# Optimization experiments

Hardware: AMD Instinct MI355X
Metric: run time of the kernel (lower is better)

Reference implementation:

```python
import jax, jax.numpy as jnp
import numpy as np

N_NODES = 50000
N_EDGES = 800000
N_GRAPHS = 64
F_IN = 128
HEADS = 4
CH = 32
HID = HEADS * CH  # 128
N_CLASSES = 10
N_LAYERS = 3
NEG_SLOPE = 0.2


def setup_inputs() -> dict:
    key = jax.random.key(0)
    ks = jax.random.split(key, 12)
    x = jax.random.normal(ks[0], (N_NODES, F_IN), dtype=jnp.float32)
    edge_index = jax.random.randint(ks[1], (2, N_EDGES), 0, N_NODES, dtype=jnp.int64)
    batch = jnp.sort(jax.random.randint(ks[2], (N_NODES,), 0, N_GRAPHS, dtype=jnp.int64))
    s = 0.1
    Wl = jax.random.normal(ks[3], (N_LAYERS, F_IN, HID), dtype=jnp.float32) * s
    Wr = jax.random.normal(ks[4], (N_LAYERS, F_IN, HID), dtype=jnp.float32) * s
    bl = jax.random.normal(ks[5], (N_LAYERS, HID), dtype=jnp.float32) * s
    br = jax.random.normal(ks[6], (N_LAYERS, HID), dtype=jnp.float32) * s
    att = jax.random.normal(ks[7], (N_LAYERS, HEADS, CH), dtype=jnp.float32) * s
    bias = jax.random.normal(ks[8], (N_LAYERS, HID), dtype=jnp.float32) * s
    lin_w = jax.random.normal(ks[9], (HID, N_CLASSES), dtype=jnp.float32) * s
    lin_b = jax.random.normal(ks[10], (N_CLASSES,), dtype=jnp.float32) * s
    return {"x": x, "edge_index": edge_index, "batch": batch, "Wl": Wl, "Wr": Wr,
            "bl": bl, "br": br, "att": att, "bias": bias, "lin_w": lin_w, "lin_b": lin_b}


def gatv2_layer(x, Wl, Wr, bl, br, att, bias, src, dst):
    # x: [N, D_in] -> out: [N, HEADS*CH]
    n = x.shape[0]
    xl = (x @ Wl + bl).reshape(n, HEADS, CH)  # source transform
    xr = (x @ Wr + br).reshape(n, HEADS, CH)  # target transform
    # GATv2 edge scores: a^T LeakyReLU(W_l x_j + W_r x_i), per head
    e = jnp.einsum('ehc,hc->eh', jax.nn.leaky_relu(xl[src] + xr[dst], NEG_SLOPE), att)  # [E, H]
    # softmax over edges sharing the same destination node
    m = jax.ops.segment_max(e, dst, num_segments=n)
    ee = jnp.exp(e - m[dst])
    denom = jax.ops.segment_sum(ee, dst, num_segments=n)
    alpha = ee / denom[dst]  # [E, H]
    out = jax.ops.segment_sum(xl[src] * alpha[:, :, None], dst, num_segments=n)  # [N, H, C]
    return out.reshape(n, HID) + bias


def reference(x, edge_index, batch, Wl, Wr, bl, br, att, bias, lin_w, lin_b):
    n = x.shape[0]
    loop = jnp.arange(n, dtype=edge_index.dtype)
    src = jnp.concatenate([edge_index[0], loop])  # self loops (PyG default)
    dst = jnp.concatenate([edge_index[1], loop])
    h = x
    for l in range(N_LAYERS):
        h = jax.nn.elu(gatv2_layer(h, Wl[l], Wr[l], bl[l], br[l], att[l], bias[l], src, dst))
    # global mean pool over graphs
    sums = jax.ops.segment_sum(h, batch, num_segments=N_GRAPHS)
    cnt = jax.ops.segment_sum(jnp.ones((n,), h.dtype), batch, num_segments=N_GRAPHS)
    pooled = sums / jnp.maximum(cnt, 1.0)[:, None]
    logits = jax.nn.elu(pooled @ lin_w + lin_b)
    return jax.nn.log_softmax(logits, axis=1)
```

## Files before the change

kernel.cpp:

```cpp
#include <hip/hip_runtime.h>
#include <hip/hip_bf16.h>
#include <math.h>

#define N_NODES 50000
#define N_EDGES 800000
#define N_GRAPHS 64
#define HID 128
#define N_CLASSES 10
#define N_LAYERS 3
#define NEG_SLOPE 0.2f

#define NB 196
#define BCAP 5120
#define ACHUNK 4096

typedef __attribute__((ext_vector_type(8))) short short8;
typedef __attribute__((ext_vector_type(4))) float f32x4;

__device__ inline ushort f2bf(float f) {
    uint u = __builtin_bit_cast(uint, f);
    u += 0x7fffu + ((u >> 16) & 1u);
    return (ushort)(u >> 16);
}
__device__ inline uint pk2bf(float a, float b) {
    return (uint)f2bf(a) | ((uint)f2bf(b) << 16);
}
__device__ inline float bflo(uint v) { return __builtin_bit_cast(float, v << 16); }
__device__ inline float bfhi(uint v) { return __builtin_bit_cast(float, v & 0xffff0000u); }


__global__ __launch_bounds__(256) void setup_kernel(
    const float* __restrict__ x, uint* __restrict__ xb, int n,
    const float* __restrict__ Wl, const float* __restrict__ Wr,
    uint* __restrict__ wt, int wtot,
    const int* __restrict__ ei, int E,
    int* __restrict__ bptr, uint* __restrict__ bbuf,
    int xqb, int wb) {
    __shared__ int hcnt[256];
    __shared__ int hexcl[256];
    __shared__ int lofs[256];
    __shared__ int delta[256];
    __shared__ uint stage[ACHUNK];
    int t = threadIdx.x;
    int blk = blockIdx.x;

    if (blk < xqb) {
        int j = blk * 256 + t;
        if (j < n * 16) {
            const float4* xp = (const float4*)x + (size_t)j * 2;
            float4 a = xp[0], b = xp[1];
            uint4 o;
            o.x = pk2bf(a.x, a.y); o.y = pk2bf(a.z, a.w);
            o.z = pk2bf(b.x, b.y); o.w = pk2bf(b.z, b.w);
            ((uint4*)xb)[j] = o;
        }
        return;
    }
    blk -= xqb;
    if (blk < wb) {
        int i = blk * 256 + t;
        if (i >= wtot) return;
        int kp = i & 63;
        int nn = (i >> 6) & 255;
        int l  = i >> 14;
        const float* W = (nn < 128) ? Wl : Wr;
        int c = nn & 127;
        wt[i] = pk2bf(W[l * 16384 + (2 * kp) * 128 + c],
                      W[l * 16384 + (2 * kp + 1) * 128 + c]);
        return;
    }
    blk -= wb;
    int total = E + n;
    int base = blk * ACHUNK;
    int cntblk = min(ACHUNK, total - base);
    hcnt[t] = 0; lofs[t] = 0;
    __syncthreads();

    uint v[16]; int bk[16];
#pragma unroll
    for (int j = 0; j < 16; ++j) {
        int e = base + j * 256 + t;
        bk[j] = -1;
        if (e < total) {
            int s, d;
            if (e < E) { s = ei[e]; d = ei[E + e]; }
            else       { s = e - E; d = e - E; }
            v[j] = ((uint)s << 16) | (uint)d;
            bk[j] = d >> 8;
            atomicAdd(&hcnt[bk[j]], 1);
        }
    }
    __syncthreads();
    int hv = hcnt[t];
    __shared__ int stmp[256];
    stmp[t] = hv;
    __syncthreads();
    for (int off = 1; off < 256; off <<= 1) {
        int u = (t >= off) ? stmp[t - off] : 0;
        __syncthreads();
        stmp[t] += u;
        __syncthreads();
    }
    hexcl[t] = stmp[t] - hv;
    __syncthreads();
#pragma unroll
    for (int j = 0; j < 16; ++j) {
        if (bk[j] >= 0) {
            int pos = hexcl[bk[j]] + atomicAdd(&lofs[bk[j]], 1);
            stage[pos] = v[j];
        }
    }
    __syncthreads();
    if (t < NB) {
        int c = hcnt[t];
        int gb = c ? atomicAdd(&bptr[t], c) : 0;
        delta[t] = t * BCAP + gb - hexcl[t];
    }
    __syncthreads();
    for (int idx = t; idx < cntblk; idx += 256) {
        uint val = stage[idx];
        int b = (val >> 8) & 0xff;
        int tgt = delta[b] + idx;
        if (tgt < (b + 1) * BCAP) bbuf[tgt] = val;
    }
}


__device__ __forceinline__ void gemm_body(
    const ushort* __restrict__ A, const ushort* __restrict__ Wt,
    const float* __restrict__ bl, const float* __restrict__ br,
    ushort* __restrict__ xlb, ushort* __restrict__ xrb, int n, int bid, int tid) {
    int wv = tid >> 6;
    int lane = tid & 63;
    int q = lane >> 4, m16 = lane & 15;
    int m0 = bid * 64;

    short8 bf[4][4];
#pragma unroll
    for (int nt = 0; nt < 4; ++nt) {
        const ushort* wp = Wt + (size_t)(wv * 64 + nt * 16 + m16) * 128 + q * 8;
#pragma unroll
        for (int ks = 0; ks < 4; ++ks) bf[nt][ks] = *(const short8*)(wp + ks * 32);
    }
    const ushort* ap[4];
#pragma unroll
    for (int mt = 0; mt < 4; ++mt) {
        int r = m0 + mt * 16 + m16;
        if (r > n - 1) r = n - 1;
        ap[mt] = A + (size_t)r * 128 + q * 8;
    }

    f32x4 z = {0.f, 0.f, 0.f, 0.f};
    f32x4 acc[4][4];
#pragma unroll
    for (int mt = 0; mt < 4; ++mt)
#pragma unroll
        for (int nt = 0; nt < 4; ++nt) acc[mt][nt] = z;

#pragma unroll
    for (int ks = 0; ks < 4; ++ks) {
        short8 af[4];
#pragma unroll
        for (int mt = 0; mt < 4; ++mt) af[mt] = *(const short8*)(ap[mt] + ks * 32);
#pragma unroll
        for (int mt = 0; mt < 4; ++mt)
#pragma unroll
            for (int nt = 0; nt < 4; ++nt)
                acc[mt][nt] = __builtin_amdgcn_mfma_f32_16x16x32_bf16(
                    bf[nt][ks], af[mt], acc[mt][nt], 0, 0, 0);
    }

    ushort* outp = (wv >= 2) ? xrb : xlb;
    const float* bx = (wv >= 2) ? br : bl;
    int fb = (wv & 1) * 64;
#pragma unroll
    for (int nt = 0; nt < 4; ++nt) {
        int fcol = fb + nt * 16 + q * 4;
        float4 b4 = *(const float4*)&bx[fcol];
#pragma unroll
        for (int mt = 0; mt < 4; ++mt) {
            int m = m0 + mt * 16 + m16;
            if (m < n) {
                ushort4 pk;
                pk.x = f2bf(acc[mt][nt][0] + b4.x);
                pk.y = f2bf(acc[mt][nt][1] + b4.y);
                pk.z = f2bf(acc[mt][nt][2] + b4.z);
                pk.w = f2bf(acc[mt][nt][3] + b4.w);
                *(ushort4*)&outp[(size_t)m * 128 + fcol] = pk;
            }
        }
    }
}

__global__ __launch_bounds__(256) void csr_gemm0_kernel(
    const int* __restrict__ bptr, const uint* __restrict__ bbuf, int n,
    int* __restrict__ row_start, int* __restrict__ ssrc,
    const ushort* __restrict__ A, const ushort* __restrict__ Wt,
    const float* __restrict__ bl, const float* __restrict__ br,
    ushort* __restrict__ xlb, ushort* __restrict__ xrb) {
    int t = threadIdx.x;
    if (blockIdx.x >= NB) {
        gemm_body(A, Wt, bl, br, xlb, xrb, n, blockIdx.x - NB, t);
        return;
    }
    int b = blockIdx.x;
    __shared__ int sb[256], h[256], hx[256], lofs[256];
    int bv = (t < NB) ? min(bptr[t], BCAP) : 0;
    sb[t] = bv;
    __syncthreads();
    for (int off = 1; off < 256; off <<= 1) {
        int u = (t >= off) ? sb[t - off] : 0;
        __syncthreads();
        sb[t] += u;
        __syncthreads();
    }
    int cnt = min(bptr[b], BCAP);
    int base = sb[b] - cnt;
    if (b == NB - 1 && t == 0) row_start[n] = sb[NB - 1];
    h[t] = 0; lofs[t] = 0;
    __syncthreads();
    const uint* bp = bbuf + (size_t)b * BCAP;
    for (int k = t; k < cnt; k += 256) atomicAdd(&h[bp[k] & 255u], 1);
    __syncthreads();
    int hv = h[t];
    hx[t] = hv;
    __syncthreads();
    for (int off = 1; off < 256; off <<= 1) {
        int u = (t >= off) ? hx[t - off] : 0;
        __syncthreads();
        hx[t] += u;
        __syncthreads();
    }
    int excl = hx[t] - hv;
    int node = (b << 8) + t;
    if (node < n) row_start[node] = base + excl;
    __syncthreads();
    h[t] = excl;
    __syncthreads();
    for (int k = t; k < cnt; k += 256) {
        uint val = bp[k];
        int dl = val & 255u;
        int pos = base + h[dl] + atomicAdd(&lofs[dl], 1);
        ssrc[pos] = (int)((val & 0xffff0000u) >> 8);
    }
}

__global__ __launch_bounds__(256) void gemm_mfma(
    const ushort* __restrict__ A, const ushort* __restrict__ Wt,
    const float* __restrict__ bl, const float* __restrict__ br,
    ushort* __restrict__ xlb, ushort* __restrict__ xrb, int n) {
    gemm_body(A, Wt, bl, br, xlb, xrb, n, blockIdx.x, threadIdx.x);
}


#define EDGE_MATH(u, c0, c1, c2, c3, e)                                  \
    {                                                                    \
        float t_;                                                        \
        c0 = bflo(u.x); c1 = bfhi(u.x); c2 = bflo(u.y); c3 = bfhi(u.y);  \
        t_ = c0 + xr0; t_ = fmaxf(t_, 0.2f * t_); e  = atx * t_;         \
        t_ = c1 + xr1; t_ = fmaxf(t_, 0.2f * t_); e += aty * t_;         \
        t_ = c2 + xr2; t_ = fmaxf(t_, 0.2f * t_); e += atz * t_;         \
        t_ = c3 + xr3; t_ = fmaxf(t_, 0.2f * t_); e += atw * t_;         \
    }

__global__ __launch_bounds__(256) void attn_kernel(
    const uint* __restrict__ xlb, const uint* __restrict__ xrb,
    const float* __restrict__ att, const float* __restrict__ bias,
    const int* __restrict__ row_start, const int* __restrict__ ssrc,
    uint* __restrict__ hout, int n) {
    int wave = threadIdx.x >> 6;
    int lane = threadIdx.x & 63;
    int half = lane >> 5;
    int l32  = lane & 31;
    int i = blockIdx.x * 4 + wave;
    if (i >= n) return;

    const char* xlB = (const char*)xlb;
    int lofs = l32 * 8;

    uint2 xru = *(const uint2*)((const char*)xrb + (size_t)i * 256 + lofs);
    float xr0 = bflo(xru.x), xr1 = bfhi(xru.x), xr2 = bflo(xru.y), xr3 = bfhi(xru.y);
    const float L2E = 1.4426950408889634f;
    float4 at = ((const float4*)att)[l32];
    float atx = at.x * L2E, aty = at.y * L2E, atz = at.z * L2E, atw = at.w * L2E;

    int p0 = row_start[i], p1 = row_start[i + 1];

    float den0 = 0.f, den1 = 0.f;
    float b00 = 0.f, b01 = 0.f, b02 = 0.f, b03 = 0.f;
    float b10 = 0.f, b11 = 0.f, b12 = 0.f, b13 = 0.f;

    int p = p0;
    for (; p + 8 <= p1; p += 8) {
        uint s0 = (uint)ssrc[p + half];
        uint s1 = (uint)ssrc[p + 2 + half];
        uint s2 = (uint)ssrc[p + 4 + half];
        uint s3 = (uint)ssrc[p + 6 + half];
        uint2 u0 = *(const uint2*)(xlB + (size_t)s0 + lofs);
        uint2 u1 = *(const uint2*)(xlB + (size_t)s1 + lofs);
        uint2 u2 = *(const uint2*)(xlB + (size_t)s2 + lofs);
        uint2 u3 = *(const uint2*)(xlB + (size_t)s3 + lofs);
        float c00, c01, c02, c03, c10, c11, c12, c13;
        float c20, c21, c22, c23, c30, c31, c32, c33;
        float e0, e1, e2, e3;
        EDGE_MATH(u0, c00, c01, c02, c03, e0);
        EDGE_MATH(u1, c10, c11, c12, c13, e1);
        EDGE_MATH(u2, c20, c21, c22, c23, e2);
        EDGE_MATH(u3, c30, c31, c32, c33, e3);
        e0 += __shfl_xor(e0, 1); e1 += __shfl_xor(e1, 1);
        e2 += __shfl_xor(e2, 1); e3 += __shfl_xor(e3, 1);
        e0 += __shfl_xor(e0, 2); e1 += __shfl_xor(e1, 2);
        e2 += __shfl_xor(e2, 2); e3 += __shfl_xor(e3, 2);
        e0 += __shfl_xor(e0, 4); e1 += __shfl_xor(e1, 4);
        e2 += __shfl_xor(e2, 4); e3 += __shfl_xor(e3, 4);
        float w0 = exp2f(e0), w1 = exp2f(e1), w2 = exp2f(e2), w3 = exp2f(e3);
        den0 += w0 + w2; den1 += w1 + w3;
        b00 += w0 * c00; b01 += w0 * c01; b02 += w0 * c02; b03 += w0 * c03;
        b10 += w1 * c10; b11 += w1 * c11; b12 += w1 * c12; b13 += w1 * c13;
        b00 += w2 * c20; b01 += w2 * c21; b02 += w2 * c22; b03 += w2 * c23;
        b10 += w3 * c30; b11 += w3 * c31; b12 += w3 * c32; b13 += w3 * c33;
    }
    if (p + 4 <= p1) {
        uint s0 = (uint)ssrc[p + half];
        uint s1 = (uint)ssrc[p + 2 + half];
        uint2 u0 = *(const uint2*)(xlB + (size_t)s0 + lofs);
        uint2 u1 = *(const uint2*)(xlB + (size_t)s1 + lofs);
        float c00, c01, c02, c03, c10, c11, c12, c13;
        float e0, e1;
        EDGE_MATH(u0, c00, c01, c02, c03, e0);
        EDGE_MATH(u1, c10, c11, c12, c13, e1);
        e0 += __shfl_xor(e0, 1); e1 += __shfl_xor(e1, 1);
        e0 += __shfl_xor(e0, 2); e1 += __shfl_xor(e1, 2);
        e0 += __shfl_xor(e0, 4); e1 += __shfl_xor(e1, 4);
        float w0 = exp2f(e0), w1 = exp2f(e1);
        den0 += w0; den1 += w1;
        b00 += w0 * c00; b01 += w0 * c01; b02 += w0 * c02; b03 += w0 * c03;
        b10 += w1 * c10; b11 += w1 * c11; b12 += w1 * c12; b13 += w1 * c13;
        p += 4;
    }
    if (p < p1) {
        int eA = p + half, eB = p + 2 + half;
        int lst = p1 - 1;
        uint s0 = (uint)ssrc[min(eA, lst)];
        uint s1 = (uint)ssrc[min(eB, lst)];
        uint2 u0 = *(const uint2*)(xlB + (size_t)s0 + lofs);
        uint2 u1 = *(const uint2*)(xlB + (size_t)s1 + lofs);
        float c00, c01, c02, c03, c10, c11, c12, c13;
        float e0, e1;
        EDGE_MATH(u0, c00, c01, c02, c03, e0);
        EDGE_MATH(u1, c10, c11, c12, c13, e1);
        e0 += __shfl_xor(e0, 1); e1 += __shfl_xor(e1, 1);
        e0 += __shfl_xor(e0, 2); e1 += __shfl_xor(e1, 2);
        e0 += __shfl_xor(e0, 4); e1 += __shfl_xor(e1, 4);
        float w0 = (eA < p1) ? exp2f(e0) : 0.f;
        float w1 = (eB < p1) ? exp2f(e1) : 0.f;
        den0 += w0; den1 += w1;
        b00 += w0 * c00; b01 += w0 * c01; b02 += w0 * c02; b03 += w0 * c03;
        b10 += w1 * c10; b11 += w1 * c11; b12 += w1 * c12; b13 += w1 * c13;
    }

    float den = den0 + den1;
    float a0 = b00 + b10, a1 = b01 + b11, a2 = b02 + b12, a3 = b03 + b13;
    den += __shfl_xor(den, 32);
    a0 += __shfl_xor(a0, 32);
    a1 += __shfl_xor(a1, 32);
    a2 += __shfl_xor(a2, 32);
    a3 += __shfl_xor(a3, 32);

    if (half == 0) {
        float inv = 1.f / den;
        float4 bi = ((const float4*)bias)[l32];
        float o0 = a0 * inv + bi.x; o0 = o0 > 0.f ? o0 : __expf(o0) - 1.f;
        float o1 = a1 * inv + bi.y; o1 = o1 > 0.f ? o1 : __expf(o1) - 1.f;
        float o2 = a2 * inv + bi.z; o2 = o2 > 0.f ? o2 : __expf(o2) - 1.f;
        float o3 = a3 * inv + bi.w; o3 = o3 > 0.f ? o3 : __expf(o3) - 1.f;
        uint2 pk;
        pk.x = pk2bf(o0, o1);
        pk.y = pk2bf(o2, o3);
        *(uint2*)((char*)hout + (size_t)i * 256 + lofs) = pk;
    }
}


__global__ __launch_bounds__(256) void pool_kernel(const uint* __restrict__ h2,
                                                   const int* __restrict__ batch, int n,
                                                   float* __restrict__ psum) {
    int g = blockIdx.x;
    int t = threadIdx.x;
    int cp = t & 63;
    int sub = (t >> 6) | (blockIdx.y << 2);
    int b, e;
    {
        int lo = 0, hi = n;
        while (lo < hi) { int mid = (lo + hi) >> 1; if (batch[mid] < g) lo = mid + 1; else hi = mid; }
        b = lo;
        lo = 0; hi = n;
        int g1 = g + 1;
        while (lo < hi) { int mid = (lo + hi) >> 1; if (batch[mid] < g1) lo = mid + 1; else hi = mid; }
        e = lo;
    }
    float a0 = 0.f, a1 = 0.f;
    for (int i = b + sub; i < e; i += 32) {
        uint u = h2[(size_t)i * 64 + cp];
        a0 += bflo(u); a1 += bfhi(u);
    }
    __shared__ float r0[256], r1[256];
    r0[t] = a0; r1[t] = a1;
    __syncthreads();
    if (t < 64) {
        float s0 = r0[t] + r0[t + 64] + r0[t + 128] + r0[t + 192];
        float s1 = r1[t] + r1[t + 64] + r1[t + 128] + r1[t + 192];
        atomicAdd(&psum[g * 128 + 2 * t], s0);
        atomicAdd(&psum[g * 128 + 2 * t + 1], s1);
    }
}

__global__ void final_kernel(const float* __restrict__ psum, const int* __restrict__ batch,
                             int n, const float* __restrict__ lw,
                             const float* __restrict__ lb, float* __restrict__ out) {
    int g = threadIdx.x;
    if (g >= N_GRAPHS) return;
    int b, e;
    {
        int lo = 0, hi = n;
        while (lo < hi) { int mid = (lo + hi) >> 1; if (batch[mid] < g) lo = mid + 1; else hi = mid; }
        b = lo;
        lo = 0; hi = n;
        int g1 = g + 1;
        while (lo < hi) { int mid = (lo + hi) >> 1; if (batch[mid] < g1) lo = mid + 1; else hi = mid; }
        e = lo;
    }
    float invc = 1.f / fmaxf((float)(e - b), 1.f);
    float z[N_CLASSES];
#pragma unroll
    for (int c = 0; c < N_CLASSES; ++c) z[c] = lb[c];
    for (int k = 0; k < 128; ++k) {
        float p = psum[g * 128 + k] * invc;
#pragma unroll
        for (int c = 0; c < N_CLASSES; ++c) z[c] += p * lw[k * N_CLASSES + c];
    }
    float mx = -1e30f;
#pragma unroll
    for (int c = 0; c < N_CLASSES; ++c) {
        z[c] = z[c] > 0.f ? z[c] : expf(z[c]) - 1.f;
        mx = fmaxf(mx, z[c]);
    }
    float s = 0.f;
#pragma unroll
    for (int c = 0; c < N_CLASSES; ++c) s += expf(z[c] - mx);
    float lse = mx + logf(s);
#pragma unroll
    for (int c = 0; c < N_CLASSES; ++c) out[g * N_CLASSES + c] = z[c] - lse;
}


extern "C" void kernel_launch(void* const* d_in, const int* in_sizes, int n_in,
                              void* d_out, int out_size, void* d_ws, size_t ws_size,
                              hipStream_t stream) {
    const float* x     = (const float*)d_in[0];
    const int*   ei    = (const int*)d_in[1];
    const int*   batch = (const int*)d_in[2];
    const float* Wl    = (const float*)d_in[3];
    const float* Wr    = (const float*)d_in[4];
    const float* bl    = (const float*)d_in[5];
    const float* br    = (const float*)d_in[6];
    const float* att   = (const float*)d_in[7];
    const float* bias  = (const float*)d_in[8];
    const float* lw    = (const float*)d_in[9];
    const float* lb    = (const float*)d_in[10];
    float* out = (float*)d_out;

    const int n = in_sizes[2];
    const int E = in_sizes[1] / 2;
    const int total_edges = E + n;

    char* ws = (char*)d_ws;
    size_t o = 0;
    auto alloc = [&](size_t bytes) -> void* {
        void* p = ws + o;
        o = (o + bytes + 255) & ~(size_t)255;
        return p;
    };
    int*    row_start = (int*)alloc((size_t)(n + 1) * 4);
    int*    bptr      = (int*)alloc((size_t)NB * 4);
    uint*   bbuf      = (uint*)alloc((size_t)NB * BCAP * 4);
    int*    ssrc      = (int*)alloc((size_t)total_edges * 4);
    ushort* xbf0      = (ushort*)alloc((size_t)n * HID * 2);
    ushort* xlb       = (ushort*)alloc((size_t)n * HID * 2);
    ushort* xrb       = (ushort*)alloc((size_t)n * HID * 2);
    ushort* hbA       = (ushort*)alloc((size_t)n * HID * 2);
    ushort* hbB       = (ushort*)alloc((size_t)n * HID * 2);
    uint*   wt        = (uint*)alloc((size_t)N_LAYERS * 256 * 64 * 4);
    float*  psum      = (float*)alloc((size_t)N_GRAPHS * HID * 4);

    hipMemsetAsync(bptr, 0, (size_t)NB * 4, stream);
    hipMemsetAsync(psum, 0, (size_t)N_GRAPHS * HID * 4, stream);

    int wtot = N_LAYERS * 256 * 64;
    int xqb = (n * 16 + 255) / 256;
    int wb  = (wtot + 255) / 256;
    int pb  = (total_edges + ACHUNK - 1) / ACHUNK;
    setup_kernel<<<xqb + wb + pb, 256, 0, stream>>>(
        x, (uint*)xbf0, n, Wl, Wr, wt, wtot, ei, E, bptr, bbuf, xqb, wb);

    int mblocks = (n + 63) / 64;
    int ablocks = (n + 3) / 4;

    csr_gemm0_kernel<<<NB + mblocks, 256, 0, stream>>>(
        bptr, bbuf, n, row_start, ssrc,
        xbf0, (const ushort*)wt, bl, br, xlb, xrb);

    attn_kernel<<<ablocks, 256, 0, stream>>>((const uint*)xlb, (const uint*)xrb,
                                             att, bias, row_start, ssrc, (uint*)hbA, n);
    gemm_mfma<<<mblocks, 256, 0, stream>>>(hbA, (const ushort*)(wt + (size_t)256 * 64),
                                           bl + HID, br + HID, xlb, xrb, n);
    attn_kernel<<<ablocks, 256, 0, stream>>>((const uint*)xlb, (const uint*)xrb,
                                             att + HID, bias + HID, row_start, ssrc,
                                             (uint*)hbB, n);
    gemm_mfma<<<mblocks, 256, 0, stream>>>(hbB, (const ushort*)(wt + (size_t)2 * 256 * 64),
                                           bl + 2 * HID, br + 2 * HID, xlb, xrb, n);
    attn_kernel<<<ablocks, 256, 0, stream>>>((const uint*)xlb, (const uint*)xrb,
                                             att + 2 * HID, bias + 2 * HID, row_start, ssrc,
                                             (uint*)hbA, n);

    pool_kernel<<<dim3(N_GRAPHS, 8), 256, 0, stream>>>((const uint*)hbA, batch, n, psum);
    final_kernel<<<1, 64, 0, stream>>>(psum, batch, n, lw, lb, out);
}
```

Measured before the change: 367.4 us.

## Store xl/xr as fp16 and do attention math in packed fp16

The GEMM epilogue now writes the source and target transforms as fp16, using packed round-toward-zero conversion instead of manual bf16 rounding. The attention kernel computes the GATv2 scores and the weighted aggregation with packed half2 arithmetic, roughly halving the VALU instructions per edge. A constant negative offset is added to each score before exp2; it cancels in the softmax but keeps the fp16 accumulators smaller. The trade-off is reduced precision and possible overflow, since the numerators are accumulated in fp16 across all neighbours.

After: 341.0 us. 7.2% less time.

```diff
diff --git a/kernel.cpp b/kernel.cpp
--- a/kernel.cpp
+++ b/kernel.cpp
@@ -16,6 +16,7 @@
 
 typedef __attribute__((ext_vector_type(8))) short short8;
 typedef __attribute__((ext_vector_type(4))) float f32x4;
+typedef __attribute__((ext_vector_type(2))) _Float16 h2;
 
 __device__ inline ushort f2bf(float f) {
     uint u = __builtin_bit_cast(uint, f);
@@ -25,8 +26,9 @@
 __device__ inline uint pk2bf(float a, float b) {
     return (uint)f2bf(a) | ((uint)f2bf(b) << 16);
 }
-__device__ inline float bflo(uint v) { return __builtin_bit_cast(float, v << 16); }
-__device__ inline float bfhi(uint v) { return __builtin_bit_cast(float, v & 0xffff0000u); }
+__device__ inline h2 pkh(float a, float b) {
+    return __builtin_bit_cast(h2, __builtin_amdgcn_cvt_pkrtz(a, b));
+}
 
 
 __global__ __launch_bounds__(256) void setup_kernel(
@@ -181,12 +183,12 @@
         for (int mt = 0; mt < 4; ++mt) {
             int m = m0 + mt * 16 + m16;
             if (m < n) {
-                ushort4 pk;
-                pk.x = f2bf(acc[mt][nt][0] + b4.x);
-                pk.y = f2bf(acc[mt][nt][1] + b4.y);
-                pk.z = f2bf(acc[mt][nt][2] + b4.z);
-                pk.w = f2bf(acc[mt][nt][3] + b4.w);
-                *(ushort4*)&outp[(size_t)m * 128 + fcol] = pk;
+                uint2 pk;
+                pk.x = __builtin_bit_cast(uint, pkh(acc[mt][nt][0] + b4.x,
+                                                    acc[mt][nt][1] + b4.y));
+                pk.y = __builtin_bit_cast(uint, pkh(acc[mt][nt][2] + b4.z,
+                                                    acc[mt][nt][3] + b4.w));
+                *(uint2*)&outp[(size_t)m * 128 + fcol] = pk;
             }
         }
     }
@@ -253,14 +255,18 @@
 }
 
 
-#define EDGE_MATH(u, c0, c1, c2, c3, e)                                  \
-    {                                                                    \
-        float t_;                                                        \
-        c0 = bflo(u.x); c1 = bfhi(u.x); c2 = bflo(u.y); c3 = bfhi(u.y);  \
-        t_ = c0 + xr0; t_ = fmaxf(t_, 0.2f * t_); e  = atx * t_;         \
-        t_ = c1 + xr1; t_ = fmaxf(t_, 0.2f * t_); e += aty * t_;         \
-        t_ = c2 + xr2; t_ = fmaxf(t_, 0.2f * t_); e += atz * t_;         \
-        t_ = c3 + xr3; t_ = fmaxf(t_, 0.2f * t_); e += atw * t_;         \
+#define SLOT(u, u01, u23, e0)                              \
+    h2 u01 = __builtin_bit_cast(h2, u.x);                  \
+    h2 u23 = __builtin_bit_cast(h2, u.y);                  \
+    float e0;                                              \
+    {                                                      \
+        h2 t01 = u01 + xr01, t23 = u23 + xr23;             \
+        t01 = __builtin_elementwise_max(t01, t01 * K02);   \
+        t23 = __builtin_elementwise_max(t23, t23 * K02);   \
+        h2 eh = EINIT;                                     \
+        eh += at01 * t01;                                  \
+        eh += at23 * t23;                                  \
+        e0 = (float)(_Float16)(eh.x + eh.y);               \
     }
 
 __global__ __launch_bounds__(256) void attn_kernel(
@@ -279,16 +285,20 @@
     int lofs = l32 * 8;
 
     uint2 xru = *(const uint2*)((const char*)xrb + (size_t)i * 256 + lofs);
-    float xr0 = bflo(xru.x), xr1 = bfhi(xru.x), xr2 = bflo(xru.y), xr3 = bfhi(xru.y);
+    h2 xr01 = __builtin_bit_cast(h2, xru.x);
+    h2 xr23 = __builtin_bit_cast(h2, xru.y);
     const float L2E = 1.4426950408889634f;
     float4 at = ((const float4*)att)[l32];
-    float atx = at.x * L2E, aty = at.y * L2E, atz = at.z * L2E, atw = at.w * L2E;
+    h2 at01 = pkh(at.x * L2E, at.y * L2E);
+    h2 at23 = pkh(at.z * L2E, at.w * L2E);
+    const h2 K02   = {(_Float16)0.2f, (_Float16)0.2f};
+    const h2 EINIT = {(_Float16)-0.5f, (_Float16)-0.5f};
 
     int p0 = row_start[i], p1 = row_start[i + 1];
 
     float den0 = 0.f, den1 = 0.f;
-    float b00 = 0.f, b01 = 0.f, b02 = 0.f, b03 = 0.f;
-    float b10 = 0.f, b11 = 0.f, b12 = 0.f, b13 = 0.f;
+    h2 aA01 = {0, 0}, aA23 = {0, 0};
+    h2 aB01 = {0, 0}, aB23 = {0, 0};
 
     int p = p0;
     for (; p + 8 <= p1; p += 8) {
@@ -300,13 +310,10 @@
         uint2 u1 = *(const uint2*)(xlB + (size_t)s1 + lofs);
         uint2 u2 = *(const uint2*)(xlB + (size_t)s2 + lofs);
         uint2 u3 = *(const uint2*)(xlB + (size_t)s3 + lofs);
-        float c00, c01, c02, c03, c10, c11, c12, c13;
-        float c20, c21, c22, c23, c30, c31, c32, c33;
-        float e0, e1, e2, e3;
-        EDGE_MATH(u0, c00, c01, c02, c03, e0);
-        EDGE_MATH(u1, c10, c11, c12, c13, e1);
-        EDGE_MATH(u2, c20, c21, c22, c23, e2);
-        EDGE_MATH(u3, c30, c31, c32, c33, e3);
+        SLOT(u0, v001, v023, e0);
+        SLOT(u1, v101, v123, e1);
+        SLOT(u2, v201, v223, e2);
+        SLOT(u3, v301, v323, e3);
         e0 += __shfl_xor(e0, 1); e1 += __shfl_xor(e1, 1);
         e2 += __shfl_xor(e2, 1); e3 += __shfl_xor(e3, 1);
         e0 += __shfl_xor(e0, 2); e1 += __shfl_xor(e1, 2);
@@ -315,27 +322,28 @@
         e2 += __shfl_xor(e2, 4); e3 += __shfl_xor(e3, 4);
         float w0 = exp2f(e0), w1 = exp2f(e1), w2 = exp2f(e2), w3 = exp2f(e3);
         den0 += w0 + w2; den1 += w1 + w3;
-        b00 += w0 * c00; b01 += w0 * c01; b02 += w0 * c02; b03 += w0 * c03;
-        b10 += w1 * c10; b11 += w1 * c11; b12 += w1 * c12; b13 += w1 * c13;
-        b00 += w2 * c20; b01 += w2 * c21; b02 += w2 * c22; b03 += w2 * c23;
-        b10 += w3 * c30; b11 += w3 * c31; b12 += w3 * c32; b13 += w3 * c33;
+        h2 wh0 = pkh(w0, w0), wh1 = pkh(w1, w1);
+        h2 wh2 = pkh(w2, w2), wh3 = pkh(w3, w3);
+        aA01 += wh0 * v001; aA23 += wh0 * v023;
+        aB01 += wh1 * v101; aB23 += wh1 * v123;
+        aA01 += wh2 * v201; aA23 += wh2 * v223;
+        aB01 += wh3 * v301; aB23 += wh3 * v323;
     }
     if (p + 4 <= p1) {
         uint s0 = (uint)ssrc[p + half];
         uint s1 = (uint)ssrc[p + 2 + half];
         uint2 u0 = *(const uint2*)(xlB + (size_t)s0 + lofs);
         uint2 u1 = *(const uint2*)(xlB + (size_t)s1 + lofs);
-        float c00, c01, c02, c03, c10, c11, c12, c13;
-        float e0, e1;
-        EDGE_MATH(u0, c00, c01, c02, c03, e0);
-        EDGE_MATH(u1, c10, c11, c12, c13, e1);
+        SLOT(u0, v001, v023, e0);
+        SLOT(u1, v101, v123, e1);
         e0 += __shfl_xor(e0, 1); e1 += __shfl_xor(e1, 1);
         e0 += __shfl_xor(e0, 2); e1 += __shfl_xor(e1, 2);
         e0 += __shfl_xor(e0, 4); e1 += __shfl_xor(e1, 4);
         float w0 = exp2f(e0), w1 = exp2f(e1);
         den0 += w0; den1 += w1;
-        b00 += w0 * c00; b01 += w0 * c01; b02 += w0 * c02; b03 += w0 * c03;
-        b10 += w1 * c10; b11 += w1 * c11; b12 += w1 * c12; b13 += w1 * c13;
+        h2 wh0 = pkh(w0, w0), wh1 = pkh(w1, w1);
+        aA01 += wh0 * v001; aA23 += wh0 * v023;
+        aB01 += wh1 * v101; aB23 += wh1 * v123;
         p += 4;
     }
     if (p < p1) {
@@ -345,22 +353,24 @@
         uint s1 = (uint)ssrc[min(eB, lst)];
         uint2 u0 = *(const uint2*)(xlB + (size_t)s0 + lofs);
         uint2 u1 = *(const uint2*)(xlB + (size_t)s1 + lofs);
-        float c00, c01, c02, c03, c10, c11, c12, c13;
-        float e0, e1;
-        EDGE_MATH(u0, c00, c01, c02, c03, e0);
-        EDGE_MATH(u1, c10, c11, c12, c13, e1);
+        SLOT(u0, v001, v023, e0);
+        SLOT(u1, v101, v123, e1);
         e0 += __shfl_xor(e0, 1); e1 += __shfl_xor(e1, 1);
         e0 += __shfl_xor(e0, 2); e1 += __shfl_xor(e1, 2);
         e0 += __shfl_xor(e0, 4); e1 += __shfl_xor(e1, 4);
         float w0 = (eA < p1) ? exp2f(e0) : 0.f;
         float w1 = (eB < p1) ? exp2f(e1) : 0.f;
         den0 += w0; den1 += w1;
-        b00 += w0 * c00; b01 += w0 * c01; b02 += w0 * c02; b03 += w0 * c03;
-        b10 += w1 * c10; b11 += w1 * c11; b12 += w1 * c12; b13 += w1 * c13;
+        h2 wh0 = pkh(w0, w0), wh1 = pkh(w1, w1);
+        aA01 += wh0 * v001; aA23 += wh0 * v023;
+        aB01 += wh1 * v101; aB23 += wh1 * v123;
     }
 
     float den = den0 + den1;
-    float a0 = b00 + b10, a1 = b01 + b11, a2 = b02 + b12, a3 = b03 + b13;
+    float a0 = (float)(_Float16)(aA01.x + aB01.x);
+    float a1 = (float)(_Float16)(aA01.y + aB01.y);
+    float a2 = (float)(_Float16)(aA23.x + aB23.x);
+    float a3 = (float)(_Float16)(aA23.y + aB23.y);
     den += __shfl_xor(den, 32);
     a0 += __shfl_xor(a0, 32);
     a1 += __shfl_xor(a1, 32);
@@ -382,7 +392,10 @@
 }
 
 
-__global__ __launch_bounds__(256) void pool_kernel(const uint* __restrict__ h2,
+__device__ inline float bflo(uint v) { return __builtin_bit_cast(float, v << 16); }
+__device__ inline float bfhi(uint v) { return __builtin_bit_cast(float, v & 0xffff0000u); }
+
+__global__ __launch_bounds__(256) void pool_kernel(const uint* __restrict__ h2v,
                                                    const int* __restrict__ batch, int n,
                                                    float* __restrict__ psum) {
     int g = blockIdx.x;
@@ -401,7 +414,7 @@
     }
     float a0 = 0.f, a1 = 0.f;
     for (int i = b + sub; i < e; i += 32) {
-        uint u = h2[(size_t)i * 64 + cp];
+        uint u = h2v[(size_t)i * 64 + cp];
         a0 += bflo(u); a1 += bfhi(u);
     }
     __shared__ float r0[256], r1[256];
```
